# Performance work log

Hardware: AMD Instinct MI355X
Metric: run time of the kernel (lower is better)

Reference implementation:

```python
import jax, jax.numpy as jnp
import numpy as np

B, T, D, H = 128, 256, 512, 256
TOP_K = 3


def _gru_dir(x, mask, w_ih, w_hh, b_ih, b_hh):
    """Unidirectional GRU (torch gate order r,z,n) with length masking.
    x: (B,T,D), mask: (B,T) bool. Returns (B,T,H) with padded steps zeroed."""
    Bn, Tn, _ = x.shape
    Hn = w_hh.shape[1]
    xg = jnp.einsum('btd,gd->btg', x, w_ih) + b_ih  # (B,T,3H) precomputed input gates

    def step(h, inp):
        xt, mt = inp  # (B,3H), (B,1)
        hg = h @ w_hh.T + b_hh
        xr, xz, xn = jnp.split(xt, 3, axis=-1)
        hr, hz, hn = jnp.split(hg, 3, axis=-1)
        r = jax.nn.sigmoid(xr + hr)
        z = jax.nn.sigmoid(xz + hz)
        n = jnp.tanh(xn + r * hn)
        h_new = (1.0 - z) * n + z * h
        h = jnp.where(mt, h_new, h)
        return h, jnp.where(mt, h_new, 0.0)

    h0 = jnp.zeros((Bn, Hn), x.dtype)
    xs = (jnp.swapaxes(xg, 0, 1), jnp.swapaxes(mask[..., None], 0, 1))
    _, out = jax.lax.scan(step, h0, xs)
    return jnp.swapaxes(out, 0, 1)


def setup_inputs() -> dict:
    key = jax.random.key(0)
    ks = jax.random.split(key, 20)
    s = 0.02
    inp = {
        'feats': jax.random.normal(ks[0], (B, T, D), jnp.float32),
        'lengths': jax.random.randint(ks[1], (B,), 1, T + 1),
        'temperature': jnp.float32(0.1),
        'w_ih_f': jax.random.normal(ks[2], (3 * H, D), jnp.float32) * s,
        'w_hh_f': jax.random.normal(ks[3], (3 * H, H), jnp.float32) * s,
        'b_ih_f': jnp.zeros((3 * H,), jnp.float32),
        'b_hh_f': jnp.zeros((3 * H,), jnp.float32),
        'w_ih_b': jax.random.normal(ks[4], (3 * H, D), jnp.float32) * s,
        'w_hh_b': jax.random.normal(ks[5], (3 * H, H), jnp.float32) * s,
        'b_ih_b': jnp.zeros((3 * H,), jnp.float32),
        'b_hh_b': jnp.zeros((3 * H,), jnp.float32),
        'w1': jax.random.normal(ks[6], (64, 2 * H), jnp.float32) * s,
        'b1': jnp.zeros((64,), jnp.float32),
        'w2': jax.random.normal(ks[7], (1, 64), jnp.float32) * s,
        'b2': jnp.zeros((1,), jnp.float32),
        'w_tens': jax.random.normal(ks[8], (11, 2 * H), jnp.float32) * s,
        'b_tens': jnp.zeros((11,), jnp.float32),
        'w_ones': jax.random.normal(ks[9], (10, 2 * H), jnp.float32) * s,
        'b_ones': jnp.zeros((10,), jnp.float32),
    }
    return inp


def _forward(feats, lengths, temperature, w_ih_f, w_hh_f, b_ih_f, b_hh_f,
             w_ih_b, w_hh_b, b_ih_b, b_hh_b, w1, b1, w2, b2,
             w_tens, b_tens, w_ones, b_ones):
    Bn, Tn, _ = feats.shape
    t_idx = jnp.arange(Tn)
    mask = t_idx[None, :] < lengths[:, None]  # (B,T)

    # forward-direction GRU
    out_f = _gru_dir(feats, mask, w_ih_f, w_hh_f, b_ih_f, b_hh_f)
    # backward-direction: reverse each sequence within its own length
    rev_idx = jnp.where(mask, lengths[:, None] - 1 - t_idx[None, :], t_idx[None, :])
    x_rev = jnp.take_along_axis(feats, rev_idx[..., None], axis=1)
    out_b_rev = _gru_dir(x_rev, mask, w_ih_b, w_hh_b, b_ih_b, b_hh_b)
    out_b = jnp.take_along_axis(out_b_rev, rev_idx[..., None], axis=1)

    output = jnp.concatenate([out_f, out_b], axis=-1)  # (B,T,2H)

    # score MLP -> (B,T)
    hmid = jax.nn.relu(jnp.einsum('bth,kh->btk', output, w1) + b1)
    scores = (jnp.einsum('btk,ok->bto', hmid, w2) + b2)[..., 0]

    # hard-concrete top-k attention
    temp = jnp.clip(temperature, 0.001, 10.0)
    logits = jnp.where(mask, scores / temp, -jnp.inf)
    probs = jax.nn.softmax(logits, axis=1)

    k_use = min(TOP_K, Tn)
    topv, topi = jax.lax.top_k(probs, k_use)  # (B,k)
    k_actual = jnp.minimum(lengths, TOP_K)
    keep = jnp.arange(k_use)[None, :] < k_actual[:, None]
    vals = jnp.where(keep, topv, 0.0)
    vsum = vals.sum(axis=1, keepdims=True)
    vnorm = jnp.where(keep, vals / jnp.maximum(vsum, 1e-8), 0.0)
    attn = jnp.zeros_like(probs).at[jnp.arange(Bn)[:, None], topi].set(vnorm)
    # fallback to uniform-over-valid if top-k mass vanished
    maskf = mask.astype(probs.dtype)
    uniform = maskf / (maskf.sum(axis=1, keepdims=True) + 1e-8)
    attn = jnp.where(vsum > 1e-8, attn, uniform)

    seq_feat = jnp.einsum('bth,bt->bh', output, attn)  # (B,2H)
    tens_logits = seq_feat @ w_tens.T + b_tens
    ones_logits = seq_feat @ w_ones.T + b_ones
    return tens_logits, ones_logits


def reference(feats, lengths, temperature, w_ih_f, w_hh_f, b_ih_f, b_hh_f,
              w_ih_b, w_hh_b, b_ih_b, b_hh_b, w1, b1, w2, b2,
              w_tens, b_tens, w_ones, b_ones):
    return _forward(feats, lengths, temperature, w_ih_f, w_hh_f, b_ih_f, b_hh_f,
                    w_ih_b, w_hh_b, b_ih_b, b_hh_b, w1, b1, w2, b2,
                    w_tens, b_tens, w_ones, b_ones)
```

## Files before the change

kernel.cpp:

```cpp
#include <hip/hip_runtime.h>
#include <cmath>

#define BB 128
#define TT 256
#define DD 512
#define HH 256
#define G3 768

typedef float f32x4 __attribute__((ext_vector_type(4)));
typedef short s16x8 __attribute__((ext_vector_type(8)));
typedef unsigned long long ull;
typedef unsigned short u16;

#define DOT2(acc, w, h) \
  asm("v_dot2_f32_f16 %0, %1, %2, %0" : "+v"(acc) : "v"(w), "v"(h))

__device__ __forceinline__ void split_bf16(float x, u16& h, u16& l)
{
  unsigned u = __float_as_uint(x);
  unsigned hr = u + 0x7fffu + ((u >> 16) & 1u);
  h = (u16)(hr >> 16);
  float hf = __uint_as_float((unsigned)h << 16);
  float lo = x - hf;
  unsigned u2 = __float_as_uint(lo);
  unsigned lr2 = u2 + 0x7fffu + ((u2 >> 16) & 1u);
  l = (u16)(lr2 >> 16);
}

__device__ __forceinline__ float bf_hl(u16 h, u16 l)
{
  return __uint_as_float((unsigned)h << 16) + __uint_as_float((unsigned)l << 16);
}

__device__ __forceinline__ u16 f32_to_f16(float x)
{
  _Float16 h = (_Float16)x;
  u16 r; __builtin_memcpy(&r, &h, 2); return r;
}

__device__ __forceinline__ float f16_to_f32(u16 v)
{
  _Float16 h; __builtin_memcpy(&h, &v, 2); return (float)h;
}

__global__ __launch_bounds__(256) void cvt_split_kernel(
    const float* __restrict__ src, u16* __restrict__ dh,
    u16* __restrict__ dl, int n8)
{
  const int i = blockIdx.x * 256 + threadIdx.x;
  if (i >= n8) return;
  const float4 v0 = *(const float4*)(src + (size_t)i * 8);
  const float4 v1 = *(const float4*)(src + (size_t)i * 8 + 4);
  float f[8] = {v0.x, v0.y, v0.z, v0.w, v1.x, v1.y, v1.z, v1.w};
  u16 hh[8], ll[8];
#pragma unroll
  for (int j = 0; j < 8; j++) split_bf16(f[j], hh[j], ll[j]);
  *(uint4*)(dh + (size_t)i * 8) = *(const uint4*)hh;
  *(uint4*)(dl + (size_t)i * 8) = *(const uint4*)ll;
}

__global__ __launch_bounds__(256) void gemm_bf3(
    const u16* __restrict__ Ah, const u16* __restrict__ Al,
    const u16* __restrict__ Wh, const u16* __restrict__ Wl,
    const float* __restrict__ bias, float* __restrict__ C,
    int M, int N, int K,
    u16* __restrict__ Crz, float* __restrict__ Cn, int split)
{
  __shared__ unsigned aH[128][20], aL[128][20], bH[128][20], bL[128][20];
  const int tid = threadIdx.x;
  const int row0 = blockIdx.y * 128, col0 = blockIdx.x * 128;
  const int wid = tid >> 6, lane = tid & 63;
  const int wm = wid >> 1, wn = wid & 1;
  const int lr = lane & 15, kq = lane >> 4;
  const int sr = tid >> 1, sh = tid & 1;

  f32x4 acc[4][4];
#pragma unroll
  for (int i = 0; i < 4; i++)
#pragma unroll
    for (int j = 0; j < 4; j++) acc[i][j] = (f32x4){0.f, 0.f, 0.f, 0.f};

  const u16* pah = Ah + (size_t)(row0 + sr) * K + sh * 16;
  const u16* pal = Al + (size_t)(row0 + sr) * K + sh * 16;
  const u16* pwh = Wh + (size_t)(col0 + sr) * K + sh * 16;
  const u16* pwl = Wl + (size_t)(col0 + sr) * K + sh * 16;
  const bool wok = (col0 + sr) < N;
  const uint4 z4 = make_uint4(0u, 0u, 0u, 0u);

  uint4 rah0 = *(const uint4*)(pah), rah1 = *(const uint4*)(pah + 8);
  uint4 ral0 = *(const uint4*)(pal), ral1 = *(const uint4*)(pal + 8);
  uint4 rbh0 = wok ? *(const uint4*)(pwh) : z4;
  uint4 rbh1 = wok ? *(const uint4*)(pwh + 8) : z4;
  uint4 rbl0 = wok ? *(const uint4*)(pwl) : z4;
  uint4 rbl1 = wok ? *(const uint4*)(pwl + 8) : z4;

  for (int k0 = 0; k0 < K; k0 += 32) {
    __syncthreads();
    ((uint4*)&aH[sr][sh * 8])[0] = rah0; ((uint4*)&aH[sr][sh * 8])[1] = rah1;
    ((uint4*)&aL[sr][sh * 8])[0] = ral0; ((uint4*)&aL[sr][sh * 8])[1] = ral1;
    ((uint4*)&bH[sr][sh * 8])[0] = rbh0; ((uint4*)&bH[sr][sh * 8])[1] = rbh1;
    ((uint4*)&bL[sr][sh * 8])[0] = rbl0; ((uint4*)&bL[sr][sh * 8])[1] = rbl1;
    __syncthreads();
    if (k0 + 32 < K) {
      rah0 = *(const uint4*)(pah + k0 + 32); rah1 = *(const uint4*)(pah + k0 + 40);
      ral0 = *(const uint4*)(pal + k0 + 32); ral1 = *(const uint4*)(pal + k0 + 40);
      rbh0 = wok ? *(const uint4*)(pwh + k0 + 32) : z4;
      rbh1 = wok ? *(const uint4*)(pwh + k0 + 40) : z4;
      rbl0 = wok ? *(const uint4*)(pwl + k0 + 32) : z4;
      rbl1 = wok ? *(const uint4*)(pwl + k0 + 40) : z4;
    }
    s16x8 ah[4], al4[4], bh4[4], bl4[4];
#pragma unroll
    for (int f = 0; f < 4; f++) {
      const int ra = wm * 64 + f * 16 + lr;
      const int rb = wn * 64 + f * 16 + lr;
      ah[f]  = *(const s16x8*)((const short*)&aH[ra][0] + kq * 8);
      al4[f] = *(const s16x8*)((const short*)&aL[ra][0] + kq * 8);
      bh4[f] = *(const s16x8*)((const short*)&bH[rb][0] + kq * 8);
      bl4[f] = *(const s16x8*)((const short*)&bL[rb][0] + kq * 8);
    }
#pragma unroll
    for (int mf = 0; mf < 4; mf++)
#pragma unroll
      for (int nf = 0; nf < 4; nf++) {
        acc[mf][nf] = __builtin_amdgcn_mfma_f32_16x16x32_bf16(ah[mf],  bh4[nf], acc[mf][nf], 0, 0, 0);
        acc[mf][nf] = __builtin_amdgcn_mfma_f32_16x16x32_bf16(ah[mf],  bl4[nf], acc[mf][nf], 0, 0, 0);
        acc[mf][nf] = __builtin_amdgcn_mfma_f32_16x16x32_bf16(al4[mf], bh4[nf], acc[mf][nf], 0, 0, 0);
      }
  }
#pragma unroll
  for (int mf = 0; mf < 4; mf++)
#pragma unroll
    for (int nf = 0; nf < 4; nf++) {
      const int c = col0 + wn * 64 + nf * 16 + lr;
      if (c < N) {
        const float bsv = bias[c];
#pragma unroll
        for (int i = 0; i < 4; i++) {
          const int r = row0 + wm * 64 + mf * 16 + kq * 4 + i;
          const float v = acc[mf][nf][i] + bsv;
          if (split) {
            if (c < 512) Crz[(size_t)r * 512 + c] = f32_to_f16(v);
            else         Cn[(size_t)r * 256 + (c - 512)] = v;
          } else {
            C[(size_t)r * N + c] = v;
          }
        }
      }
    }
}

__global__ __launch_bounds__(256) void wcvt_kernel(
    const float* __restrict__ whh_f, const float* __restrict__ whh_b,
    unsigned* __restrict__ wf16)
{
  const int gid = blockIdx.x * 256 + threadIdx.x;
  if (gid >= 2 * 512 * 192) return;
  const int dir = gid / (512 * 192);
  const int rem = gid % (512 * 192);
  const int th = rem / 192;
  const int q  = rem % 192;
  const int kc = th >> 8, u = th & 255;
  const int g = q / 64, j = q % 64;
  const int k = kc * 128 + 2 * j;
  const float* w = dir ? whh_b : whh_f;
  const float w0 = w[((size_t)g * HH + u) * HH + k];
  const float w1v = w[((size_t)g * HH + u) * HH + k + 1];
  _Float16 a = (_Float16)w0, b = (_Float16)w1v;
  u16 ua, ub;
  __builtin_memcpy(&ua, &a, 2);
  __builtin_memcpy(&ub, &b, 2);
  wf16[gid] = (unsigned)ua | ((unsigned)ub << 16);
}

__global__ __launch_bounds__(512, 1) void gru_solo_kernel(
    const u16* __restrict__ xgRZ_f, const float* __restrict__ xgN_f,
    const u16* __restrict__ xgRZ_b, const float* __restrict__ xgN_b,
    const unsigned* __restrict__ wf16,
    const float* __restrict__ bhh_f, const float* __restrict__ bhh_b,
    const int* __restrict__ lengths,
    u16* __restrict__ Oh, u16* __restrict__ Ol, int mode)
{
  const int tid = threadIdx.x;
  const int bx = blockIdx.x;
  const int dir = (mode < 0) ? (bx >> 7) : mode;
  const int batch = (mode < 0) ? (bx & 127) : bx;
  const int u = tid >> 1, kc = tid & 1;
  const int len = lengths[batch];
  const u16*   xgRZ = dir ? xgRZ_b : xgRZ_f;
  const float* xgN  = dir ? xgN_b  : xgN_f;
  const float* bhh  = dir ? bhh_b  : bhh_f;

  __shared__ uint4 h16[2][32];
  if (tid < 32) h16[0][tid] = make_uint4(0u, 0u, 0u, 0u);

  uint4 wR[16], wZ[16], wN[16];
  {
    const uint4* wb = (const uint4*)(wf16 + (size_t)(dir * 512 + kc * 256 + u) * 192);
#pragma unroll
    for (int i = 0; i < 16; i++) wR[i] = wb[i];
#pragma unroll
    for (int i = 0; i < 16; i++) wZ[i] = wb[16 + i];
#pragma unroll
    for (int i = 0; i < 16; i++) wN[i] = wb[32 + i];
  }
  const float br = bhh[u], bz = bhh[HH + u], bn = bhh[2 * HH + u];
  float hreg = 0.f;
  __syncthreads();

  int p = dir ? (len - 1) : 0;
  const int ps = dir ? -1 : 1;
  float xr = 0.f, xz = 0.f, xn = 0.f;
  if (kc == 0) {
    const size_t rz = ((size_t)batch * TT + p) * 512;
    xr = f16_to_f32(xgRZ[rz + u]);
    xz = f16_to_f32(xgRZ[rz + 256 + u]);
    xn = xgN[((size_t)batch * TT + p) * 256 + u];
  }
  u16 oh_p = 0, ol_p = 0;
  size_t oi_p = 0;

  for (int t = 0; t < len; t++) {
    if (kc == 0 && t > 0) { Oh[oi_p] = oh_p; Ol[oi_p] = ol_p; }
    float nr = 0.f, nz = 0.f, nn = 0.f;
    if (kc == 0 && t + 1 < len) {
      const size_t rz = ((size_t)batch * TT + p + ps) * 512;
      nr = f16_to_f32(xgRZ[rz + u]);
      nz = f16_to_f32(xgRZ[rz + 256 + u]);
      nn = xgN[((size_t)batch * TT + p + ps) * 256 + u];
    }
    float aR = 0.f, aZ = 0.f, aN = 0.f;
    const uint4* hb = &h16[t & 1][kc << 4];
#pragma unroll
    for (int c = 0; c < 16; c++) {
      const uint4 hv = hb[c];
      DOT2(aR, wR[c].x, hv.x); DOT2(aZ, wZ[c].x, hv.x); DOT2(aN, wN[c].x, hv.x);
      DOT2(aR, wR[c].y, hv.y); DOT2(aZ, wZ[c].y, hv.y); DOT2(aN, wN[c].y, hv.y);
      DOT2(aR, wR[c].z, hv.z); DOT2(aZ, wZ[c].z, hv.z); DOT2(aN, wN[c].z, hv.z);
      DOT2(aR, wR[c].w, hv.w); DOT2(aZ, wZ[c].w, hv.w); DOT2(aN, wN[c].w, hv.w);
    }
    aR += __shfl_xor(aR, 1);
    aZ += __shfl_xor(aZ, 1);
    aN += __shfl_xor(aN, 1);
    if (kc == 0) {
      const float er = __expf(-(xr + aR + br));
      const float r = __builtin_amdgcn_rcpf(1.f + er);
      const float ez = __expf(-(xz + aZ + bz));
      const float z = __builtin_amdgcn_rcpf(1.f + ez);
      const float xa = xn + r * (aN + bn);
      const float e2 = __expf(-2.f * xa);
      const float th = (1.f - e2) * __builtin_amdgcn_rcpf(1.f + e2);
      const float hn = (1.f - z) * th + z * hreg;
      hreg = hn;
      ((_Float16*)h16[(t + 1) & 1])[u] = (_Float16)hn;
      split_bf16(hn, oh_p, ol_p);
      oi_p = ((size_t)batch * TT + p) * (2 * HH) + dir * HH + u;
    }
    __syncthreads();
    p += ps; xr = nr; xz = nz; xn = nn;
  }
  if (kc == 0 && len > 0) { Oh[oi_p] = oh_p; Ol[oi_p] = ol_p; }
}

__global__ __launch_bounds__(256) void score2_kernel(
    const float* __restrict__ hmid, const float* __restrict__ w2,
    const float* __restrict__ b2, const int* __restrict__ lengths,
    float* __restrict__ scores)
{
  const int wv = threadIdx.x >> 6, lane = threadIdx.x & 63;
  const int bt = blockIdx.x * 4 + wv;
  const int b = bt >> 8, t = bt & 255;
  float v = 0.f;
  if (t < lengths[b]) {
    float hv = fmaxf(hmid[(size_t)bt * 64 + lane], 0.f);
    v = hv * w2[lane];
#pragma unroll
    for (int o = 32; o > 0; o >>= 1) v += __shfl_down(v, o);
    v += b2[0];
  }
  if (lane == 0) scores[bt] = v;
}

__global__ __launch_bounds__(256) void attn_kernel(
    const float* __restrict__ scores,
    const u16* __restrict__ Oh, const u16* __restrict__ Ol,
    const float* __restrict__ temp_ptr, const int* __restrict__ lengths,
    float* __restrict__ seq_feat)
{
  const int b = blockIdx.x;
  const int t = threadIdx.x;
  const int len = lengths[b];
  float temp = fminf(fmaxf(temp_ptr[0], 0.001f), 10.0f);
  __shared__ float red[256];
  __shared__ int redi[256];
  __shared__ float topv[3]; __shared__ int topi[3];
  __shared__ float vn[3]; __shared__ float vsum_s;
  const bool valid = t < len;
  float logit = valid ? scores[b * TT + t] / temp : -INFINITY;
  red[t] = logit; __syncthreads();
  for (int s = 128; s > 0; s >>= 1) {
    if (t < s) red[t] = fmaxf(red[t], red[t + s]);
    __syncthreads();
  }
  float mx = red[0]; __syncthreads();
  float e = valid ? expf(logit - mx) : 0.f;
  red[t] = e; __syncthreads();
  for (int s = 128; s > 0; s >>= 1) {
    if (t < s) red[t] += red[t + s];
    __syncthreads();
  }
  float sum = red[0]; __syncthreads();
  float myp = e / sum;
  for (int it = 0; it < 3; it++) {
    red[t] = myp; redi[t] = t; __syncthreads();
    for (int s = 128; s > 0; s >>= 1) {
      if (t < s) {
        float v2 = red[t + s]; int i2 = redi[t + s];
        if (v2 > red[t] || (v2 == red[t] && i2 < redi[t])) { red[t] = v2; redi[t] = i2; }
      }
      __syncthreads();
    }
    if (t == 0) { topv[it] = red[0]; topi[it] = redi[0]; }
    __syncthreads();
    if (t == topi[it]) myp = -1.f;
    __syncthreads();
  }
  if (t == 0) {
    int k_act = len < 3 ? len : 3;
    float vsum = 0.f;
    for (int jj = 0; jj < 3; jj++) if (jj < k_act) vsum += topv[jj];
    vsum_s = vsum;
    float denom = fmaxf(vsum, 1e-8f);
    for (int jj = 0; jj < 3; jj++) vn[jj] = (jj < k_act) ? topv[jj] / denom : 0.f;
  }
  __syncthreads();
  if (vsum_s > 1e-8f) {
    for (int hh = t; hh < 2 * HH; hh += 256) {
      float s = 0.f;
      for (int jj = 0; jj < 3; jj++) {
        const size_t oi = ((size_t)b * TT + topi[jj]) * (2 * HH) + hh;
        s += vn[jj] * bf_hl(Oh[oi], Ol[oi]);
      }
      seq_feat[b * 2 * HH + hh] = s;
    }
  } else {
    float inv = 1.f / ((float)len + 1e-8f);
    for (int hh = t; hh < 2 * HH; hh += 256) {
      float s = 0.f;
      for (int tt2 = 0; tt2 < len; tt2++) {
        const size_t oi = ((size_t)b * TT + tt2) * (2 * HH) + hh;
        s += bf_hl(Oh[oi], Ol[oi]);
      }
      seq_feat[b * 2 * HH + hh] = s * inv;
    }
  }
}

__global__ __launch_bounds__(256) void head_kernel(
    const float* __restrict__ seq_feat,
    const float* __restrict__ w_tens, const float* __restrict__ b_tens,
    const float* __restrict__ w_ones, const float* __restrict__ b_ones,
    float* __restrict__ d_out)
{
  const int b = blockIdx.x;
  const int lane = threadIdx.x & 63, wv = threadIdx.x >> 6;
  const float* sf = seq_feat + (size_t)b * 2 * HH;
  for (int o = wv; o < 21; o += 4) {
    const float* wr = (o < 11) ? (w_tens + (size_t)o * 2 * HH)
                               : (w_ones + (size_t)(o - 11) * 2 * HH);
    float s = 0.f;
    for (int e2 = lane; e2 < 2 * HH; e2 += 64) s += sf[e2] * wr[e2];
#pragma unroll
    for (int off2 = 32; off2 > 0; off2 >>= 1) s += __shfl_down(s, off2);
    if (lane == 0) {
      if (o < 11) d_out[b * 11 + o] = s + b_tens[o];
      else d_out[BB * 11 + b * 10 + (o - 11)] = s + b_ones[o - 11];
    }
  }
}

extern "C" void kernel_launch(void* const* d_in, const int* in_sizes, int n_in,
                              void* d_out, int out_size, void* d_ws, size_t ws_size,
                              hipStream_t stream)
{
  const float* feats       = (const float*)d_in[0];
  const int*   lengths     = (const int*)d_in[1];
  const float* temperature = (const float*)d_in[2];
  const float* w_ih_f = (const float*)d_in[3];
  const float* w_hh_f = (const float*)d_in[4];
  const float* b_ih_f = (const float*)d_in[5];
  const float* b_hh_f = (const float*)d_in[6];
  const float* w_ih_b = (const float*)d_in[7];
  const float* w_hh_b = (const float*)d_in[8];
  const float* b_ih_b = (const float*)d_in[9];
  const float* b_hh_b = (const float*)d_in[10];
  const float* w1 = (const float*)d_in[11];
  const float* b1 = (const float*)d_in[12];
  const float* w2 = (const float*)d_in[13];
  const float* b2 = (const float*)d_in[14];
  const float* w_tens = (const float*)d_in[15];
  const float* b_tens = (const float*)d_in[16];
  const float* w_ones = (const float*)d_in[17];
  const float* b_ones = (const float*)d_in[18];
  float* out = (float*)d_out;

  const int    M       = BB * TT;
  const size_t xgrz_sz = (size_t)M * 512 * 2;
  const size_t xgn_sz  = (size_t)M * 256 * 4;
  const size_t opl_sz  = (size_t)M * 2 * HH * 2;
  const size_t wgru_sz = (size_t)2 * 512 * 192 * 4;
  const size_t wihpl   = (size_t)G3 * DD * 2;
  const size_t w1pl    = (size_t)64 * 2 * HH * 2;
  char* ws = (char*)d_ws;

  u16*   xgRZ_f = (u16*)ws;
  float* xgN_f  = (float*)(ws + xgrz_sz);
  u16*   xgRZ_b = (u16*)(ws + xgrz_sz + xgn_sz);
  float* xgN_b  = (float*)(ws + 2 * xgrz_sz + xgn_sz);
  u16*   Oh     = (u16*)(ws + 2 * xgrz_sz + 2 * xgn_sz);
  u16*   Ol     = (u16*)(ws + 2 * xgrz_sz + 2 * xgn_sz + opl_sz);
  char*  wreg   = ws + 2 * xgrz_sz + 2 * xgn_sz + 2 * opl_sz;
  unsigned* wgru = (unsigned*)wreg;
  u16* Wfh = (u16*)(wreg + wgru_sz);
  u16* Wfl = (u16*)(wreg + wgru_sz + wihpl);
  u16* Wbh = (u16*)(wreg + wgru_sz + 2 * wihpl);
  u16* Wbl = (u16*)(wreg + wgru_sz + 3 * wihpl);
  u16* W1h = (u16*)(wreg + wgru_sz + 4 * wihpl);
  u16* W1l = (u16*)(wreg + wgru_sz + 4 * wihpl + w1pl);
  u16* Ah  = Oh;
  u16* Al  = Ol;
  float* hmid     = (float*)ws;
  float* scores   = hmid + (size_t)M * 64;
  float* seq_feat = scores + M;

  wcvt_kernel<<<768, 256, 0, stream>>>(w_hh_f, w_hh_b, wgru);
  cvt_split_kernel<<<M * DD / 8 / 256, 256, 0, stream>>>(feats, Ah, Al, M * DD / 8);
  cvt_split_kernel<<<G3 * DD / 8 / 256, 256, 0, stream>>>(w_ih_f, Wfh, Wfl, G3 * DD / 8);
  cvt_split_kernel<<<G3 * DD / 8 / 256, 256, 0, stream>>>(w_ih_b, Wbh, Wbl, G3 * DD / 8);
  cvt_split_kernel<<<16, 256, 0, stream>>>(w1, W1h, W1l, 64 * 2 * HH / 8);
  gemm_bf3<<<dim3(6, 256), 256, 0, stream>>>(
      Ah, Al, Wfh, Wfl, b_ih_f, nullptr, M, G3, DD, xgRZ_f, xgN_f, 1);
  gemm_bf3<<<dim3(6, 256), 256, 0, stream>>>(
      Ah, Al, Wbh, Wbl, b_ih_b, nullptr, M, G3, DD, xgRZ_b, xgN_b, 1);
  gru_solo_kernel<<<256, 512, 0, stream>>>(
      xgRZ_f, xgN_f, xgRZ_b, xgN_b, wgru, b_hh_f, b_hh_b, lengths, Oh, Ol, -1);
  gemm_bf3<<<dim3(1, 256), 256, 0, stream>>>(
      Oh, Ol, W1h, W1l, b1, hmid, M, 64, 2 * HH, nullptr, nullptr, 0);
  score2_kernel<<<M / 4, 256, 0, stream>>>(hmid, w2, b2, lengths, scores);
  attn_kernel<<<BB, 256, 0, stream>>>(scores, Oh, Ol, temperature, lengths, seq_feat);
  head_kernel<<<BB, 256, 0, stream>>>(seq_feat, w_tens, b_tens, w_ones, b_ones, out);
}
```

Before: 766.4 us.

## Pair longest and shortest sequences per GRU block using a sorted schedule

Adds a small kernel that ranks batch entries by length, then runs the recurrent GRU with each block handling two sequences, the longest paired with the shortest, in one direction. This halves the block count from 256 to 128 and shares the register-resident recurrent weights across two sequences per step, balancing work so each block runs roughly the max length. The cost is more instructions and registers per step while both sequences are active, plus one extra tiny launch.

Measured after the change: 835.1 us. 9.0% more time.

```diff
diff --git a/kernel.cpp b/kernel.cpp
--- a/kernel.cpp
+++ b/kernel.cpp
@@ -173,26 +173,44 @@
   wf16[gid] = (unsigned)ua | ((unsigned)ub << 16);
 }
 
-__global__ __launch_bounds__(512, 1) void gru_solo_kernel(
+__global__ void sched_kernel(const int* __restrict__ lengths,
+                             int* __restrict__ order_b)
+{
+  const int b = threadIdx.x;
+  if (b < BB) {
+    const int L = lengths[b];
+    int rank = 0;
+    for (int j = 0; j < BB; j++) {
+      const int Lj = lengths[j];
+      rank += (Lj > L) || (Lj == L && j < b);
+    }
+    order_b[rank] = b;
+  }
+}
+
+__global__ __launch_bounds__(512, 1) void gru_duo2_kernel(
     const u16* __restrict__ xgRZ_f, const float* __restrict__ xgN_f,
     const u16* __restrict__ xgRZ_b, const float* __restrict__ xgN_b,
     const unsigned* __restrict__ wf16,
     const float* __restrict__ bhh_f, const float* __restrict__ bhh_b,
-    const int* __restrict__ lengths,
-    u16* __restrict__ Oh, u16* __restrict__ Ol, int mode)
+    const int* __restrict__ lengths, const int* __restrict__ order_b,
+    u16* __restrict__ Oh, u16* __restrict__ Ol)
 {
   const int tid = threadIdx.x;
   const int bx = blockIdx.x;
-  const int dir = (mode < 0) ? (bx >> 7) : mode;
-  const int batch = (mode < 0) ? (bx & 127) : bx;
+  const int dir = bx >> 6;
+  const int q = bx & 63;
+  const int bX = order_b[q];
+  const int bY = order_b[127 - q];
   const int u = tid >> 1, kc = tid & 1;
-  const int len = lengths[batch];
+  const int lenX = lengths[bX];
+  const int lenY = lengths[bY];
   const u16*   xgRZ = dir ? xgRZ_b : xgRZ_f;
   const float* xgN  = dir ? xgN_b  : xgN_f;
   const float* bhh  = dir ? bhh_b  : bhh_f;
 
-  __shared__ uint4 h16[2][32];
-  if (tid < 32) h16[0][tid] = make_uint4(0u, 0u, 0u, 0u);
+  __shared__ uint4 h16[2][2][32];
+  if (tid < 64) ((uint4*)h16)[tid] = make_uint4(0u, 0u, 0u, 0u);
 
   uint4 wR[16], wZ[16], wN[16];
   {
@@ -205,61 +223,119 @@
     for (int i = 0; i < 16; i++) wN[i] = wb[32 + i];
   }
   const float br = bhh[u], bz = bhh[HH + u], bn = bhh[2 * HH + u];
-  float hreg = 0.f;
+  float hregX = 0.f, hregY = 0.f;
   __syncthreads();
 
-  int p = dir ? (len - 1) : 0;
+  int pX = dir ? (lenX - 1) : 0;
+  int pY = dir ? (lenY - 1) : 0;
   const int ps = dir ? -1 : 1;
-  float xr = 0.f, xz = 0.f, xn = 0.f;
+  float xrX = 0.f, xzX = 0.f, xnX = 0.f, xrY = 0.f, xzY = 0.f, xnY = 0.f;
   if (kc == 0) {
-    const size_t rz = ((size_t)batch * TT + p) * 512;
-    xr = f16_to_f32(xgRZ[rz + u]);
-    xz = f16_to_f32(xgRZ[rz + 256 + u]);
-    xn = xgN[((size_t)batch * TT + p) * 256 + u];
-  }
-  u16 oh_p = 0, ol_p = 0;
-  size_t oi_p = 0;
-
-  for (int t = 0; t < len; t++) {
-    if (kc == 0 && t > 0) { Oh[oi_p] = oh_p; Ol[oi_p] = ol_p; }
-    float nr = 0.f, nz = 0.f, nn = 0.f;
-    if (kc == 0 && t + 1 < len) {
-      const size_t rz = ((size_t)batch * TT + p + ps) * 512;
-      nr = f16_to_f32(xgRZ[rz + u]);
-      nz = f16_to_f32(xgRZ[rz + 256 + u]);
-      nn = xgN[((size_t)batch * TT + p + ps) * 256 + u];
-    }
-    float aR = 0.f, aZ = 0.f, aN = 0.f;
-    const uint4* hb = &h16[t & 1][kc << 4];
-#pragma unroll
-    for (int c = 0; c < 16; c++) {
-      const uint4 hv = hb[c];
-      DOT2(aR, wR[c].x, hv.x); DOT2(aZ, wZ[c].x, hv.x); DOT2(aN, wN[c].x, hv.x);
-      DOT2(aR, wR[c].y, hv.y); DOT2(aZ, wZ[c].y, hv.y); DOT2(aN, wN[c].y, hv.y);
-      DOT2(aR, wR[c].z, hv.z); DOT2(aZ, wZ[c].z, hv.z); DOT2(aN, wN[c].z, hv.z);
-      DOT2(aR, wR[c].w, hv.w); DOT2(aZ, wZ[c].w, hv.w); DOT2(aN, wN[c].w, hv.w);
-    }
-    aR += __shfl_xor(aR, 1);
-    aZ += __shfl_xor(aZ, 1);
-    aN += __shfl_xor(aN, 1);
+    const size_t rzX = ((size_t)bX * TT + pX) * 512;
+    xrX = f16_to_f32(xgRZ[rzX + u]);
+    xzX = f16_to_f32(xgRZ[rzX + 256 + u]);
+    xnX = xgN[((size_t)bX * TT + pX) * 256 + u];
+    const size_t rzY = ((size_t)bY * TT + pY) * 512;
+    xrY = f16_to_f32(xgRZ[rzY + u]);
+    xzY = f16_to_f32(xgRZ[rzY + 256 + u]);
+    xnY = xgN[((size_t)bY * TT + pY) * 256 + u];
+  }
+  u16 ohX = 0, olX = 0, ohY = 0, olY = 0;
+  size_t oiX = 0, oiY = 0;
+  bool pdX = false, pdY = false;
+
+  for (int t = 0; t < lenX; t++) {
+    const bool doY = t < lenY;
     if (kc == 0) {
-      const float er = __expf(-(xr + aR + br));
-      const float r = __builtin_amdgcn_rcpf(1.f + er);
-      const float ez = __expf(-(xz + aZ + bz));
-      const float z = __builtin_amdgcn_rcpf(1.f + ez);
-      const float xa = xn + r * (aN + bn);
-      const float e2 = __expf(-2.f * xa);
-      const float th = (1.f - e2) * __builtin_amdgcn_rcpf(1.f + e2);
-      const float hn = (1.f - z) * th + z * hreg;
-      hreg = hn;
-      ((_Float16*)h16[(t + 1) & 1])[u] = (_Float16)hn;
-      split_bf16(hn, oh_p, ol_p);
-      oi_p = ((size_t)batch * TT + p) * (2 * HH) + dir * HH + u;
-    }
-    __syncthreads();
-    p += ps; xr = nr; xz = nz; xn = nn;
-  }
-  if (kc == 0 && len > 0) { Oh[oi_p] = oh_p; Ol[oi_p] = ol_p; }
+      if (pdX) { Oh[oiX] = ohX; Ol[oiX] = olX; pdX = false; }
+      if (pdY) { Oh[oiY] = ohY; Ol[oiY] = olY; pdY = false; }
+    }
+    float nrX = 0.f, nzX = 0.f, nnX = 0.f, nrY = 0.f, nzY = 0.f, nnY = 0.f;
+    if (kc == 0 && t + 1 < lenX) {
+      const size_t rz = ((size_t)bX * TT + pX + ps) * 512;
+      nrX = f16_to_f32(xgRZ[rz + u]);
+      nzX = f16_to_f32(xgRZ[rz + 256 + u]);
+      nnX = xgN[((size_t)bX * TT + pX + ps) * 256 + u];
+    }
+    if (kc == 0 && t + 1 < lenY) {
+      const size_t rz = ((size_t)bY * TT + pY + ps) * 512;
+      nrY = f16_to_f32(xgRZ[rz + u]);
+      nzY = f16_to_f32(xgRZ[rz + 256 + u]);
+      nnY = xgN[((size_t)bY * TT + pY + ps) * 256 + u];
+    }
+    float aRX = 0.f, aZX = 0.f, aNX = 0.f;
+    float aRY = 0.f, aZY = 0.f, aNY = 0.f;
+    const uint4* hbX = &h16[t & 1][0][kc << 4];
+    const uint4* hbY = &h16[t & 1][1][kc << 4];
+    if (doY) {
+#pragma unroll
+      for (int c = 0; c < 16; c++) {
+        const uint4 hx = hbX[c];
+        const uint4 hy = hbY[c];
+        DOT2(aRX, wR[c].x, hx.x); DOT2(aZX, wZ[c].x, hx.x); DOT2(aNX, wN[c].x, hx.x);
+        DOT2(aRY, wR[c].x, hy.x); DOT2(aZY, wZ[c].x, hy.x); DOT2(aNY, wN[c].x, hy.x);
+        DOT2(aRX, wR[c].y, hx.y); DOT2(aZX, wZ[c].y, hx.y); DOT2(aNX, wN[c].y, hx.y);
+        DOT2(aRY, wR[c].y, hy.y); DOT2(aZY, wZ[c].y, hy.y); DOT2(aNY, wN[c].y, hy.y);
+        DOT2(aRX, wR[c].z, hx.z); DOT2(aZX, wZ[c].z, hx.z); DOT2(aNX, wN[c].z, hx.z);
+        DOT2(aRY, wR[c].z, hy.z); DOT2(aZY, wZ[c].z, hy.z); DOT2(aNY, wN[c].z, hy.z);
+        DOT2(aRX, wR[c].w, hx.w); DOT2(aZX, wZ[c].w, hx.w); DOT2(aNX, wN[c].w, hx.w);
+        DOT2(aRY, wR[c].w, hy.w); DOT2(aZY, wZ[c].w, hy.w); DOT2(aNY, wN[c].w, hy.w);
+      }
+    } else {
+#pragma unroll
+      for (int c = 0; c < 16; c++) {
+        const uint4 hx = hbX[c];
+        DOT2(aRX, wR[c].x, hx.x); DOT2(aZX, wZ[c].x, hx.x); DOT2(aNX, wN[c].x, hx.x);
+        DOT2(aRX, wR[c].y, hx.y); DOT2(aZX, wZ[c].y, hx.y); DOT2(aNX, wN[c].y, hx.y);
+        DOT2(aRX, wR[c].z, hx.z); DOT2(aZX, wZ[c].z, hx.z); DOT2(aNX, wN[c].z, hx.z);
+        DOT2(aRX, wR[c].w, hx.w); DOT2(aZX, wZ[c].w, hx.w); DOT2(aNX, wN[c].w, hx.w);
+      }
+    }
+    aRX += __shfl_xor(aRX, 1); aZX += __shfl_xor(aZX, 1); aNX += __shfl_xor(aNX, 1);
+    if (doY) {
+      aRY += __shfl_xor(aRY, 1); aZY += __shfl_xor(aZY, 1); aNY += __shfl_xor(aNY, 1);
+    }
+    if (kc == 0) {
+      {
+        const float er = __expf(-(xrX + aRX + br));
+        const float r = __builtin_amdgcn_rcpf(1.f + er);
+        const float ez = __expf(-(xzX + aZX + bz));
+        const float z = __builtin_amdgcn_rcpf(1.f + ez);
+        const float xa = xnX + r * (aNX + bn);
+        const float e2 = __expf(-2.f * xa);
+        const float th = (1.f - e2) * __builtin_amdgcn_rcpf(1.f + e2);
+        const float hn = (1.f - z) * th + z * hregX;
+        hregX = hn;
+        ((_Float16*)&h16[(t + 1) & 1][0][0])[u] = (_Float16)hn;
+        split_bf16(hn, ohX, olX);
+        oiX = ((size_t)bX * TT + pX) * (2 * HH) + dir * HH + u;
+        pdX = true;
+      }
+      if (doY) {
+        const float er = __expf(-(xrY + aRY + br));
+        const float r = __builtin_amdgcn_rcpf(1.f + er);
+        const float ez = __expf(-(xzY + aZY + bz));
+        const float z = __builtin_amdgcn_rcpf(1.f + ez);
+        const float xa = xnY + r * (aNY + bn);
+        const float e2 = __expf(-2.f * xa);
+        const float th = (1.f - e2) * __builtin_amdgcn_rcpf(1.f + e2);
+        const float hn = (1.f - z) * th + z * hregY;
+        hregY = hn;
+        ((_Float16*)&h16[(t + 1) & 1][1][0])[u] = (_Float16)hn;
+        split_bf16(hn, ohY, olY);
+        oiY = ((size_t)bY * TT + pY) * (2 * HH) + dir * HH + u;
+        pdY = true;
+      }
+    }
+    __syncthreads();
+    pX += ps; pY += ps;
+    xrX = nrX; xzX = nzX; xnX = nnX;
+    xrY = nrY; xzY = nzY; xnY = nnY;
+  }
+  if (kc == 0) {
+    if (pdX) { Oh[oiX] = ohX; Ol[oiX] = olX; }
+    if (pdY) { Oh[oiY] = ohY; Ol[oiY] = olY; }
+  }
 }
 
 __global__ __launch_bounds__(256) void score2_kernel(
@@ -427,6 +503,7 @@
   u16* Wbl = (u16*)(wreg + wgru_sz + 3 * wihpl);
   u16* W1h = (u16*)(wreg + wgru_sz + 4 * wihpl);
   u16* W1l = (u16*)(wreg + wgru_sz + 4 * wihpl + w1pl);
+  int* order_b = (int*)(wreg + wgru_sz + 4 * wihpl + 2 * w1pl);
   u16* Ah  = Oh;
   u16* Al  = Ol;
   float* hmid     = (float*)ws;
@@ -434,6 +511,7 @@
   float* seq_feat = scores + M;
 
   wcvt_kernel<<<768, 256, 0, stream>>>(w_hh_f, w_hh_b, wgru);
+  sched_kernel<<<1, 128, 0, stream>>>(lengths, order_b);
   cvt_split_kernel<<<M * DD / 8 / 256, 256, 0, stream>>>(feats, Ah, Al, M * DD / 8);
   cvt_split_kernel<<<G3 * DD / 8 / 256, 256, 0, stream>>>(w_ih_f, Wfh, Wfl, G3 * DD / 8);
   cvt_split_kernel<<<G3 * DD / 8 / 256, 256, 0, stream>>>(w_ih_b, Wbh, Wbl, G3 * DD / 8);
@@ -442,8 +520,9 @@
       Ah, Al, Wfh, Wfl, b_ih_f, nullptr, M, G3, DD, xgRZ_f, xgN_f, 1);
   gemm_bf3<<<dim3(6, 256), 256, 0, stream>>>(
       Ah, Al, Wbh, Wbl, b_ih_b, nullptr, M, G3, DD, xgRZ_b, xgN_b, 1);
-  gru_solo_kernel<<<256, 512, 0, stream>>>(
-      xgRZ_f, xgN_f, xgRZ_b, xgN_b, wgru, b_hh_f, b_hh_b, lengths, Oh, Ol, -1);
+  gru_duo2_kernel<<<128, 512, 0, stream>>>(
+      xgRZ_f, xgN_f, xgRZ_b, xgN_b, wgru, b_hh_f, b_hh_b, lengths, order_b,
+      Oh, Ol);
   gemm_bf3<<<dim3(1, 256), 256, 0, stream>>>(
       Oh, Ol, W1h, W1l, b1, hmid, M, 64, 2 * HH, nullptr, nullptr, 0);
   score2_kernel<<<M / 4, 256, 0, stream>>>(hmid, w2, b2, lengths, scores);
```
